# Optimization experiments

Hardware: AMD Instinct MI355X
Metric: run time of the kernel (lower is better)

The kernel has to match this reference:

```python
import jax, jax.numpy as jnp
import numpy as np

D_MODEL = 1024
NUM_HEADS = 16
D_K = D_MODEL // NUM_HEADS


def setup_inputs() -> dict:
    key = jax.random.key(0)
    ks = jax.random.split(key, 9)
    s = 1.0 / np.sqrt(D_MODEL)
    x = jax.random.normal(ks[0], (4, 2048, D_MODEL), dtype=jnp.float32)
    Wq = jax.random.uniform(ks[1], (D_MODEL, D_MODEL), jnp.float32, -s, s)
    bq = jax.random.uniform(ks[2], (D_MODEL,), jnp.float32, -s, s)
    Wk = jax.random.uniform(ks[3], (D_MODEL, D_MODEL), jnp.float32, -s, s)
    bk = jax.random.uniform(ks[4], (D_MODEL,), jnp.float32, -s, s)
    Wv = jax.random.uniform(ks[5], (D_MODEL, D_MODEL), jnp.float32, -s, s)
    bv = jax.random.uniform(ks[6], (D_MODEL,), jnp.float32, -s, s)
    Wo = jax.random.uniform(ks[7], (D_MODEL, D_MODEL), jnp.float32, -s, s)
    bo = jax.random.uniform(ks[8], (D_MODEL,), jnp.float32, -s, s)
    return {"x": x, "Wq": Wq, "bq": bq, "Wk": Wk, "bk": bk,
            "Wv": Wv, "bv": bv, "Wo": Wo, "bo": bo}


def reference(x, Wq, bq, Wk, bk, Wv, bv, Wo, bo):
    B, S, _ = x.shape
    # Linear projections (torch Linear: x @ W.T + b)
    q = x @ Wq.T + bq
    k = x @ Wk.T + bk
    v = x @ Wv.T + bv
    # [B, H, S, d_k]
    q = q.reshape(B, S, NUM_HEADS, D_K).transpose(0, 2, 1, 3)
    k = k.reshape(B, S, NUM_HEADS, D_K).transpose(0, 2, 1, 3)
    v = v.reshape(B, S, NUM_HEADS, D_K).transpose(0, 2, 1, 3)
    score = jnp.einsum('bhqd,bhkd->bhqk', q, k) / jnp.sqrt(jnp.float32(D_K))
    causal = jnp.tril(jnp.ones((S, S), dtype=bool))  # True = keep
    score = jnp.where(causal[None, None], score, -jnp.inf)
    attn = jax.nn.softmax(score, axis=-1)
    out = jnp.einsum('bhqk,bhkd->bhqd', attn, v)
    out = out.transpose(0, 2, 1, 3).reshape(B, S, D_MODEL)
    return out @ Wo.T + bo
```

## Files before the change

kernel.cpp:

```cpp
#include <hip/hip_runtime.h>
#include <hip/hip_bf16.h>
#include <stdint.h>

#define D_MODEL 1024
#define SEQ     2048
#define BATCH   4
#define NHEAD   16
#define DKH     64
#define MTOT    (BATCH * SEQ)

typedef __bf16 bf16x8 __attribute__((ext_vector_type(8)));
typedef __bf16 bf16x4 __attribute__((ext_vector_type(4)));
typedef float  floatx4 __attribute__((ext_vector_type(4)));
typedef short  s16x4  __attribute__((ext_vector_type(4)));

#define GLOAD_LDS16(gp, lp)                                            \
    __builtin_amdgcn_global_load_lds(                                  \
        (const __attribute__((address_space(1))) unsigned int*)(gp),   \
        (__attribute__((address_space(3))) unsigned int*)(lp), 16, 0, 0)

#define MFMA16(a, b, c) __builtin_amdgcn_mfma_f32_16x16x32_bf16(a, b, c, 0, 0, 0)

#if __has_builtin(__builtin_amdgcn_exp2f)
#define EXP2(x) __builtin_amdgcn_exp2f(x)
#else
#define EXP2(x) exp2f(x)
#endif

static __device__ __forceinline__ floatx4 pv_mfma(s16x4 a, s16x4 b, floatx4 c)
{
#if __has_builtin(__builtin_amdgcn_mfma_f32_16x16x16bf16_1k)
    return __builtin_amdgcn_mfma_f32_16x16x16bf16_1k(a, b, c, 0, 0, 0);
#else
    asm("v_mfma_f32_16x16x16_bf16 %0, %1, %2, %0" : "+v"(c) : "v"(a), "v"(b));
    return c;
#endif
}

__global__ __launch_bounds__(256)
void cvt_x_kernel(const float* __restrict__ src, __bf16* __restrict__ dst)
{
    const int i = (blockIdx.x * 256 + threadIdx.x) * 4;
    floatx4 v = *(const floatx4*)(src + i);
    bf16x4 o;
    o[0] = (__bf16)v[0]; o[1] = (__bf16)v[1]; o[2] = (__bf16)v[2]; o[3] = (__bf16)v[3];
    *(bf16x4*)(dst + i) = o;
}

__global__ __launch_bounds__(256)
void cvt_w3_kernel(const float* __restrict__ Wq, const float* __restrict__ Wk,
                   const float* __restrict__ Wv, __bf16* __restrict__ Wcat)
{
    const int z = blockIdx.y;
    const float* src = (z == 0) ? Wq : ((z == 1) ? Wk : Wv);
    const int i = (blockIdx.x * 256 + threadIdx.x) * 4;
    floatx4 v = *(const floatx4*)(src + i);
    bf16x4 o;
    o[0] = (__bf16)v[0]; o[1] = (__bf16)v[1]; o[2] = (__bf16)v[2]; o[3] = (__bf16)v[3];
    *(bf16x4*)(Wcat + (size_t)z * (D_MODEL * D_MODEL) + i) = o;
}

__global__ __launch_bounds__(256)
void qkv_gemm_kernel(const __bf16* __restrict__ xb, const __bf16* __restrict__ Wcat,
                     const float* __restrict__ bq, const float* __restrict__ bk,
                     const float* __restrict__ bv,
                     __bf16* __restrict__ Q, __bf16* __restrict__ K,
                     __bf16* __restrict__ Vt)
{
    __shared__ __align__(16) char smem_raw[128 * 136 * 2];
    __bf16* As = (__bf16*)smem_raw;
    __bf16* Bs = (__bf16*)(smem_raw + 8192);
    __bf16* Cs = (__bf16*)smem_raw;

    const int t    = threadIdx.x;
    const int w    = t >> 6, l = t & 63, quad = l >> 4, r16 = l & 15;
    const int wm   = w & 1, wn = w >> 1;
    const int m0   = blockIdx.y * 128;
    const int n0   = blockIdx.x * 128;
    const int z    = n0 >> 10;
    const float* bias = (z == 0) ? bq : ((z == 1) ? bk : bv);
    __bf16* outQK     = (z == 0) ? Q  : K;
    const float scale = (z == 0) ? 0.18033688011112042f : 1.0f;

    floatx4 acc[4][4];
#pragma unroll
    for (int i = 0; i < 4; ++i)
#pragma unroll
        for (int j = 0; j < 4; ++j) acc[i][j] = (floatx4){0.f, 0.f, 0.f, 0.f};

    const int c0 = t, c1 = t + 256;
    const __bf16* Ag0 = xb   + (size_t)(m0 + (c0 >> 2)) * 1024 + (c0 & 3) * 8;
    const __bf16* Ag1 = xb   + (size_t)(m0 + (c1 >> 2)) * 1024 + (c1 & 3) * 8;
    const __bf16* Bg0 = Wcat + (size_t)(n0 + (c0 >> 2)) * 1024 + (c0 & 3) * 8;
    const __bf16* Bg1 = Wcat + (size_t)(n0 + (c1 >> 2)) * 1024 + (c1 & 3) * 8;
    unsigned int* lAs = (unsigned int*)As;
    unsigned int* lBs = (unsigned int*)Bs;

    for (int k0 = 0; k0 < 1024; k0 += 32) {
        __syncthreads();
        GLOAD_LDS16(Ag0 + k0, lAs + c0 * 4);
        GLOAD_LDS16(Ag1 + k0, lAs + c1 * 4);
        GLOAD_LDS16(Bg0 + k0, lBs + c0 * 4);
        GLOAD_LDS16(Bg1 + k0, lBs + c1 * 4);
        __syncthreads();

        bf16x8 af[4], bfm[4];
#pragma unroll
        for (int i = 0; i < 4; ++i)
            af[i] = *(const bf16x8*)&As[(wm * 64 + i * 16 + r16) * 32 + quad * 8];
#pragma unroll
        for (int j = 0; j < 4; ++j)
            bfm[j] = *(const bf16x8*)&Bs[(wn * 64 + j * 16 + r16) * 32 + quad * 8];
#pragma unroll
        for (int i = 0; i < 4; ++i)
#pragma unroll
            for (int j = 0; j < 4; ++j)
                acc[i][j] = MFMA16(af[i], bfm[j], acc[i][j]);
    }

    __syncthreads();

    if (z == 2) {
#pragma unroll
        for (int i = 0; i < 4; ++i) {
            const int mb = wm * 64 + i * 16 + quad * 4;
#pragma unroll
            for (int j = 0; j < 4; ++j) {
                const int nl = wn * 64 + j * 16 + r16;
                const float bb = bias[(n0 + nl) & 1023];
                bf16x4 p4;
#pragma unroll
                for (int r = 0; r < 4; ++r) p4[r] = (__bf16)(acc[i][j][r] + bb);
                *(bf16x4*)&Cs[nl * 136 + mb] = p4;
            }
        }
    } else {
#pragma unroll
        for (int i = 0; i < 4; ++i) {
            const int mb = wm * 64 + i * 16 + quad * 4;
#pragma unroll
            for (int j = 0; j < 4; ++j) {
                const int nl = wn * 64 + j * 16 + r16;
                const float bb = bias[(n0 + nl) & 1023];
#pragma unroll
                for (int r = 0; r < 4; ++r)
                    Cs[(mb + r) * 136 + nl] =
                        (__bf16)((acc[i][j][r] + bb) * scale);
            }
        }
    }
    __syncthreads();

    const int b  = m0 >> 11;
    if (z == 2) {
#pragma unroll
        for (int k = 0; k < 8; ++k) {
            const int nl = (t >> 4) + k * 16;
            const int ml = (t & 15) * 8;
            bf16x8 row = *(const bf16x8*)&Cs[nl * 136 + ml];
            const int f = (n0 + nl) & 1023, h = f >> 6, d = f & 63;
            const int s = (m0 & 2047) + ml;
            *(bf16x8*)&Vt[((size_t)((b * 16 + h) * 64 + d) << 11) + s] = row;
        }
    } else {
#pragma unroll
        for (int k = 0; k < 8; ++k) {
            const int ml = (t >> 4) + k * 16;
            const int nl = (t & 15) * 8;
            bf16x8 row = *(const bf16x8*)&Cs[ml * 136 + nl];
            const int f = (n0 + nl) & 1023, h = f >> 6, d = f & 63;
            const int s = (m0 & 2047) + ml;
            *(bf16x8*)&outQK[((size_t)(b * 16 + h) << 17) + ((size_t)s << 6) + d]
                = row;
        }
    }
}

__global__ __launch_bounds__(256)
void out_gemm_kernel(const __bf16* __restrict__ A, const __bf16* __restrict__ Wob,
                     const float* __restrict__ bo, float* __restrict__ out)
{
    __shared__ __align__(16) __bf16 As[128 * 32];
    __shared__ __align__(16) __bf16 Bs[128 * 32];

    const int t    = threadIdx.x;
    const int w    = t >> 6, l = t & 63, quad = l >> 4, r16 = l & 15;
    const int wm   = w & 1, wn = w >> 1;
    const int m0   = blockIdx.y * 128;
    const int n0   = blockIdx.x * 128;

    floatx4 acc[4][4];
#pragma unroll
    for (int i = 0; i < 4; ++i)
#pragma unroll
        for (int j = 0; j < 4; ++j) acc[i][j] = (floatx4){0.f, 0.f, 0.f, 0.f};

    const int c0 = t, c1 = t + 256;
    const __bf16* Ag0 = A   + (size_t)(m0 + (c0 >> 2)) * 1024 + (c0 & 3) * 8;
    const __bf16* Ag1 = A   + (size_t)(m0 + (c1 >> 2)) * 1024 + (c1 & 3) * 8;
    const __bf16* Bg0 = Wob + (size_t)(n0 + (c0 >> 2)) * 1024 + (c0 & 3) * 8;
    const __bf16* Bg1 = Wob + (size_t)(n0 + (c1 >> 2)) * 1024 + (c1 & 3) * 8;
    unsigned int* lAs = (unsigned int*)As;
    unsigned int* lBs = (unsigned int*)Bs;

    for (int k0 = 0; k0 < 1024; k0 += 32) {
        __syncthreads();
        GLOAD_LDS16(Ag0 + k0, lAs + c0 * 4);
        GLOAD_LDS16(Ag1 + k0, lAs + c1 * 4);
        GLOAD_LDS16(Bg0 + k0, lBs + c0 * 4);
        GLOAD_LDS16(Bg1 + k0, lBs + c1 * 4);
        __syncthreads();

        bf16x8 af[4], bfm[4];
#pragma unroll
        for (int i = 0; i < 4; ++i)
            af[i] = *(const bf16x8*)&As[(wm * 64 + i * 16 + r16) * 32 + quad * 8];
#pragma unroll
        for (int j = 0; j < 4; ++j)
            bfm[j] = *(const bf16x8*)&Bs[(wn * 64 + j * 16 + r16) * 32 + quad * 8];
#pragma unroll
        for (int i = 0; i < 4; ++i)
#pragma unroll
            for (int j = 0; j < 4; ++j)
                acc[i][j] = MFMA16(af[i], bfm[j], acc[i][j]);
    }

#pragma unroll
    for (int i = 0; i < 4; ++i) {
        const int mg = m0 + wm * 64 + i * 16 + quad * 4;
#pragma unroll
        for (int j = 0; j < 4; ++j) {
            const int ng = n0 + wn * 64 + j * 16 + r16;
            const float bb = bo[ng];
#pragma unroll
            for (int r = 0; r < 4; ++r)
                out[(size_t)(mg + r) * 1024 + ng] = acc[i][j][r] + bb;
        }
    }
}

__global__ __launch_bounds__(512, 4)
void attn_kernel(const __bf16* __restrict__ Qg, const __bf16* __restrict__ Kg,
                 const __bf16* __restrict__ Vtg, __bf16* __restrict__ O)
{
    __shared__ __align__(16) __bf16 Ks[2][64 * 72];
    __shared__ __align__(16) __bf16 Vs[2][64 * 72];

    const int t    = threadIdx.x;
    const int w    = t >> 6, l = t & 63, quad = l >> 4, r16 = l & 15;
    const int bh   = blockIdx.x;
    const int qb   = blockIdx.y;
    const int qa   = 15 - qb;
    const size_t base = (size_t)bh * SEQ * DKH;
    const int g    = w >> 2;
    const int d0   = 2 * qa + g;
    const int d1   = 2 * qb + g;
    const int nkt  = 2 * qa + 2;
    const int row0 = qa * 128 + w * 16;
    const int row1 = qb * 128 + w * 16;

    const s16x4 ones16 = {(short)0x3F80, (short)0x3F80,
                          (short)0x3F80, (short)0x3F80};

    bf16x8 qf[2][2];
    qf[0][0] = *(const bf16x8*)&Qg[base + (size_t)(row0 + r16) * 64 + quad * 8];
    qf[0][1] = *(const bf16x8*)&Qg[base + (size_t)(row0 + r16) * 64 + 32 + quad * 8];
    qf[1][0] = *(const bf16x8*)&Qg[base + (size_t)(row1 + r16) * 64 + quad * 8];
    qf[1][1] = *(const bf16x8*)&Qg[base + (size_t)(row1 + r16) * 64 + 32 + quad * 8];

    floatx4 o[2][4];
#pragma unroll
    for (int mi = 0; mi < 2; ++mi)
#pragma unroll
        for (int j = 0; j < 4; ++j) o[mi][j] = (floatx4){0.f, 0.f, 0.f, 0.f};
    floatx4 osum[2];
    osum[0] = (floatx4){0.f, 0.f, 0.f, 0.f};
    osum[1] = (floatx4){0.f, 0.f, 0.f, 0.f};

    const int srow = t >> 3;
    const int sg   = (t & 7) * 8;

    bf16x8 pk = *(const bf16x8*)&Kg[base + (size_t)srow * 64 + sg];
    bf16x8 pv = *(const bf16x8*)&Vtg[base + (size_t)srow * 2048 + sg];

    for (int kt = 0; kt < nkt; ++kt) {
        __bf16* ks = Ks[kt & 1];
        __bf16* vs = Vs[kt & 1];
        *(bf16x8*)&ks[srow * 72 + sg] = pk;
        *(bf16x8*)&vs[srow * 72 + sg] = pv;
        if (kt + 1 < nkt) {
            pk = *(const bf16x8*)&Kg[base + (size_t)((kt + 1) * 64 + srow) * 64 + sg];
            pv = *(const bf16x8*)&Vtg[base + (size_t)srow * 2048 + (kt + 1) * 64 + sg];
        }
        __syncthreads();

        const bool a0 = (kt <= d0), a1 = (kt <= d1);
        if (a0) {
            __builtin_amdgcn_s_setprio(1);
            bf16x8 kf[4][2];
#pragma unroll
            for (int j = 0; j < 4; ++j) {
                kf[j][0] = *(const bf16x8*)&ks[(j * 16 + r16) * 72 + quad * 8];
                kf[j][1] = *(const bf16x8*)&ks[(j * 16 + r16) * 72 + 32 + quad * 8];
            }
#pragma unroll
            for (int j = 0; j < 4; ++j) {
                floatx4 z0 = (floatx4){0.f, 0.f, 0.f, 0.f};
                floatx4 z1 = (floatx4){0.f, 0.f, 0.f, 0.f};
                z0 = MFMA16(kf[j][0], qf[0][0], z0);
                z0 = MFMA16(kf[j][1], qf[0][1], z0);
                if (a1) {
                    z1 = MFMA16(kf[j][0], qf[1][0], z1);
                    z1 = MFMA16(kf[j][1], qf[1][1], z1);
                }

                const int kg = kt * 64 + j * 16 + quad * 4;
                bf16x4 pb0, pb1;
                if (kt < d0) {
#pragma unroll
                    for (int r = 0; r < 4; ++r)
                        pb0[r] = (__bf16)EXP2(z0[r]);
                } else {
                    const int qg0 = row0 + r16;
#pragma unroll
                    for (int r = 0; r < 4; ++r) {
                        float p = 0.f;
                        if (kg + r <= qg0) p = EXP2(z0[r]);
                        pb0[r] = (__bf16)p;
                    }
                }
                s16x4 pa0 = __builtin_bit_cast(s16x4, pb0);
                s16x4 pa1;
                if (a1) {
                    if (kt < d1) {
#pragma unroll
                        for (int r = 0; r < 4; ++r)
                            pb1[r] = (__bf16)EXP2(z1[r]);
                    } else {
                        const int qg1 = row1 + r16;
#pragma unroll
                        for (int r = 0; r < 4; ++r) {
                            float p = 0.f;
                            if (kg + r <= qg1) p = EXP2(z1[r]);
                            pb1[r] = (__bf16)p;
                        }
                    }
                    pa1 = __builtin_bit_cast(s16x4, pb1);
                }
                osum[0] = pv_mfma(pa0, ones16, osum[0]);
                if (a1) osum[1] = pv_mfma(pa1, ones16, osum[1]);
#pragma unroll
                for (int jd = 0; jd < 4; ++jd) {
                    const s16x4 vv =
                        *(const s16x4*)&vs[(jd * 16 + r16) * 72 + j * 16 + quad * 4];
                    o[0][jd] = pv_mfma(pa0, vv, o[0][jd]);
                    if (a1) o[1][jd] = pv_mfma(pa1, vv, o[1][jd]);
                }
            }
            __builtin_amdgcn_s_setprio(0);
        }
    }

    const int b = bh >> 4, h = bh & 15;
#pragma unroll
    for (int mi = 0; mi < 2; ++mi) {
        const int rowb = (mi == 0) ? row0 : row1;
#pragma unroll
        for (int r = 0; r < 4; ++r) {
            const int qrow = rowb + quad * 4 + r;
            const float inv = 1.f / osum[mi][r];
#pragma unroll
            for (int jd = 0; jd < 4; ++jd) {
                const int d = jd * 16 + r16;
                O[((size_t)(b * SEQ + qrow) * D_MODEL) + h * 64 + d] =
                    (__bf16)(o[mi][jd][r] * inv);
            }
        }
    }
}

extern "C" void kernel_launch(void* const* d_in, const int* in_sizes, int n_in,
                              void* d_out, int out_size, void* d_ws, size_t ws_size,
                              hipStream_t stream)
{
    (void)in_sizes; (void)n_in; (void)out_size; (void)ws_size;
    const float* x  = (const float*)d_in[0];
    const float* Wq = (const float*)d_in[1];
    const float* bq = (const float*)d_in[2];
    const float* Wk = (const float*)d_in[3];
    const float* bk = (const float*)d_in[4];
    const float* Wv = (const float*)d_in[5];
    const float* bv = (const float*)d_in[6];
    const float* Wo = (const float*)d_in[7];
    const float* bo = (const float*)d_in[8];
    float* out = (float*)d_out;

    const size_t n_elem = (size_t)MTOT * D_MODEL;
    const int    w_n    = D_MODEL * D_MODEL;
    __bf16* Qb  = (__bf16*)d_out;
    __bf16* xb  = Qb + n_elem;
    __bf16* Kb   = (__bf16*)d_ws;
    __bf16* Vtb  = Kb + n_elem;
    __bf16* Ab   = Vtb + n_elem;
    __bf16* Wcat = Ab;
    __bf16* Wob  = Kb;

    cvt_x_kernel<<<MTOT * D_MODEL / 1024, 256, 0, stream>>>(x, xb);
    cvt_w3_kernel<<<dim3(w_n / 1024, 3), 256, 0, stream>>>(Wq, Wk, Wv, Wcat);
    qkv_gemm_kernel<<<dim3(24, 64), 256, 0, stream>>>(xb, Wcat, bq, bk, bv,
                                                      Qb, Kb, Vtb);
    attn_kernel<<<dim3(64, 8), 512, 0, stream>>>(Qb, Kb, Vtb, Ab);
    cvt_x_kernel<<<w_n / 1024, 256, 0, stream>>>(Wo, Wob);
    out_gemm_kernel<<<dim3(8, 64), 256, 0, stream>>>(Ab, Wob, bo, out);
}
```

Measured before the change: 267.7 us.

## Split attention blocks into 256-thread halves with two-tile-ahead K/V prefetch

The attention kernel now launches twice as many 256-thread blocks, each covering one 64-row half of a paired causal query tile (qa, qb), instead of 512-thread blocks covering both halves. Each block loops only up to its own diagonal, which removes the idle iterations the second half-group of waves spent waiting in the old design. K/V staging now has each thread load two rows and prefetch two tiles ahead in registers, to hide global latency with fewer threads. The trade-off is more register pressure and less K/V reuse across waves, since each tile is loaded by twice as many blocks.

```diff
diff --git a/kernel.cpp b/kernel.cpp
--- a/kernel.cpp
+++ b/kernel.cpp
@@ -239,7 +239,7 @@
     }
 }
 
-__global__ __launch_bounds__(512, 4)
+__global__ __launch_bounds__(256, 4)
 void attn_kernel(const __bf16* __restrict__ Qg, const __bf16* __restrict__ Kg,
                  const __bf16* __restrict__ Vtg, __bf16* __restrict__ O)
 {
@@ -249,15 +249,15 @@
     const int t    = threadIdx.x;
     const int w    = t >> 6, l = t & 63, quad = l >> 4, r16 = l & 15;
     const int bh   = blockIdx.x;
-    const int qb   = blockIdx.y;
-    const int qa   = 15 - qb;
+    const int y    = blockIdx.y;
+    const int p    = y >> 1, half = y & 1;
+    const int qa   = 15 - p, qb = p;
     const size_t base = (size_t)bh * SEQ * DKH;
-    const int g    = w >> 2;
-    const int d0   = 2 * qa + g;
-    const int d1   = 2 * qb + g;
-    const int nkt  = 2 * qa + 2;
-    const int row0 = qa * 128 + w * 16;
-    const int row1 = qb * 128 + w * 16;
+    const int d0   = 2 * qa + half;
+    const int d1   = 2 * qb + half;
+    const int nkt  = d0 + 1;
+    const int row0 = qa * 128 + half * 64 + w * 16;
+    const int row1 = qb * 128 + half * 64 + w * 16;
 
     const s16x4 ones16 = {(short)0x3F80, (short)0x3F80,
                           (short)0x3F80, (short)0x3F80};
@@ -280,85 +280,100 @@
     const int srow = t >> 3;
     const int sg   = (t & 7) * 8;
 
-    bf16x8 pk = *(const bf16x8*)&Kg[base + (size_t)srow * 64 + sg];
-    bf16x8 pv = *(const bf16x8*)&Vtg[base + (size_t)srow * 2048 + sg];
-
-    for (int kt = 0; kt < nkt; ++kt) {
+    bf16x8 ka[2], va[2], kb[2], vb[2];
+    ka[0] = *(const bf16x8*)&Kg[base + (size_t)srow * 64 + sg];
+    ka[1] = *(const bf16x8*)&Kg[base + (size_t)(32 + srow) * 64 + sg];
+    va[0] = *(const bf16x8*)&Vtg[base + (size_t)srow * 2048 + sg];
+    va[1] = *(const bf16x8*)&Vtg[base + (size_t)(32 + srow) * 2048 + sg];
+    kb[0] = *(const bf16x8*)&Kg[base + (size_t)(64 + srow) * 64 + sg];
+    kb[1] = *(const bf16x8*)&Kg[base + (size_t)(96 + srow) * 64 + sg];
+    vb[0] = *(const bf16x8*)&Vtg[base + (size_t)srow * 2048 + 64 + sg];
+    vb[1] = *(const bf16x8*)&Vtg[base + (size_t)(32 + srow) * 2048 + 64 + sg];
+
+    auto do_tile = [&](const int kt, bf16x8* pk, bf16x8* pv) {
         __bf16* ks = Ks[kt & 1];
         __bf16* vs = Vs[kt & 1];
-        *(bf16x8*)&ks[srow * 72 + sg] = pk;
-        *(bf16x8*)&vs[srow * 72 + sg] = pv;
-        if (kt + 1 < nkt) {
-            pk = *(const bf16x8*)&Kg[base + (size_t)((kt + 1) * 64 + srow) * 64 + sg];
-            pv = *(const bf16x8*)&Vtg[base + (size_t)srow * 2048 + (kt + 1) * 64 + sg];
+        *(bf16x8*)&ks[srow * 72 + sg] = pk[0];
+        *(bf16x8*)&ks[(32 + srow) * 72 + sg] = pk[1];
+        *(bf16x8*)&vs[srow * 72 + sg] = pv[0];
+        *(bf16x8*)&vs[(32 + srow) * 72 + sg] = pv[1];
+        if (kt + 2 < nkt) {
+            const int kr = (kt + 2) * 64;
+            pk[0] = *(const bf16x8*)&Kg[base + (size_t)(kr + srow) * 64 + sg];
+            pk[1] = *(const bf16x8*)&Kg[base + (size_t)(kr + 32 + srow) * 64 + sg];
+            pv[0] = *(const bf16x8*)&Vtg[base + (size_t)srow * 2048 + kr + sg];
+            pv[1] = *(const bf16x8*)&Vtg[base + (size_t)(32 + srow) * 2048 + kr + sg];
         }
         __syncthreads();
 
-        const bool a0 = (kt <= d0), a1 = (kt <= d1);
-        if (a0) {
-            __builtin_amdgcn_s_setprio(1);
-            bf16x8 kf[4][2];
-#pragma unroll
-            for (int j = 0; j < 4; ++j) {
-                kf[j][0] = *(const bf16x8*)&ks[(j * 16 + r16) * 72 + quad * 8];
-                kf[j][1] = *(const bf16x8*)&ks[(j * 16 + r16) * 72 + 32 + quad * 8];
-            }
-#pragma unroll
-            for (int j = 0; j < 4; ++j) {
-                floatx4 z0 = (floatx4){0.f, 0.f, 0.f, 0.f};
-                floatx4 z1 = (floatx4){0.f, 0.f, 0.f, 0.f};
-                z0 = MFMA16(kf[j][0], qf[0][0], z0);
-                z0 = MFMA16(kf[j][1], qf[0][1], z0);
-                if (a1) {
-                    z1 = MFMA16(kf[j][0], qf[1][0], z1);
-                    z1 = MFMA16(kf[j][1], qf[1][1], z1);
+        const bool a1 = (kt <= d1);
+        __builtin_amdgcn_s_setprio(1);
+        bf16x8 kf[4][2];
+#pragma unroll
+        for (int j = 0; j < 4; ++j) {
+            kf[j][0] = *(const bf16x8*)&ks[(j * 16 + r16) * 72 + quad * 8];
+            kf[j][1] = *(const bf16x8*)&ks[(j * 16 + r16) * 72 + 32 + quad * 8];
+        }
+#pragma unroll
+        for (int j = 0; j < 4; ++j) {
+            floatx4 z0 = (floatx4){0.f, 0.f, 0.f, 0.f};
+            floatx4 z1 = (floatx4){0.f, 0.f, 0.f, 0.f};
+            z0 = MFMA16(kf[j][0], qf[0][0], z0);
+            z0 = MFMA16(kf[j][1], qf[0][1], z0);
+            if (a1) {
+                z1 = MFMA16(kf[j][0], qf[1][0], z1);
+                z1 = MFMA16(kf[j][1], qf[1][1], z1);
+            }
+
+            const int kg = kt * 64 + j * 16 + quad * 4;
+            bf16x4 pb0, pb1;
+            if (kt < d0) {
+#pragma unroll
+                for (int r = 0; r < 4; ++r)
+                    pb0[r] = (__bf16)EXP2(z0[r]);
+            } else {
+                const int qg0 = row0 + r16;
+#pragma unroll
+                for (int r = 0; r < 4; ++r) {
+                    float pp = 0.f;
+                    if (kg + r <= qg0) pp = EXP2(z0[r]);
+                    pb0[r] = (__bf16)pp;
                 }
-
-                const int kg = kt * 64 + j * 16 + quad * 4;
-                bf16x4 pb0, pb1;
-                if (kt < d0) {
+            }
+            s16x4 pa0 = __builtin_bit_cast(s16x4, pb0);
+            s16x4 pa1;
+            if (a1) {
+                if (kt < d1) {
 #pragma unroll
                     for (int r = 0; r < 4; ++r)
-                        pb0[r] = (__bf16)EXP2(z0[r]);
+                        pb1[r] = (__bf16)EXP2(z1[r]);
                 } else {
-                    const int qg0 = row0 + r16;
+                    const int qg1 = row1 + r16;
 #pragma unroll
                     for (int r = 0; r < 4; ++r) {
-                        float p = 0.f;
-                        if (kg + r <= qg0) p = EXP2(z0[r]);
-                        pb0[r] = (__bf16)p;
+                        float pp = 0.f;
+                        if (kg + r <= qg1) pp = EXP2(z1[r]);
+                        pb1[r] = (__bf16)pp;
                     }
                 }
-                s16x4 pa0 = __builtin_bit_cast(s16x4, pb0);
-                s16x4 pa1;
-                if (a1) {
-                    if (kt < d1) {
-#pragma unroll
-                        for (int r = 0; r < 4; ++r)
-                            pb1[r] = (__bf16)EXP2(z1[r]);
-                    } else {
-                        const int qg1 = row1 + r16;
-#pragma unroll
-                        for (int r = 0; r < 4; ++r) {
-                            float p = 0.f;
-                            if (kg + r <= qg1) p = EXP2(z1[r]);
-                            pb1[r] = (__bf16)p;
-                        }
-                    }
-                    pa1 = __builtin_bit_cast(s16x4, pb1);
-                }
-                osum[0] = pv_mfma(pa0, ones16, osum[0]);
-                if (a1) osum[1] = pv_mfma(pa1, ones16, osum[1]);
-#pragma unroll
-                for (int jd = 0; jd < 4; ++jd) {
-                    const s16x4 vv =
-                        *(const s16x4*)&vs[(jd * 16 + r16) * 72 + j * 16 + quad * 4];
-                    o[0][jd] = pv_mfma(pa0, vv, o[0][jd]);
-                    if (a1) o[1][jd] = pv_mfma(pa1, vv, o[1][jd]);
-                }
-            }
-            __builtin_amdgcn_s_setprio(0);
-        }
+                pa1 = __builtin_bit_cast(s16x4, pb1);
+            }
+            osum[0] = pv_mfma(pa0, ones16, osum[0]);
+            if (a1) osum[1] = pv_mfma(pa1, ones16, osum[1]);
+#pragma unroll
+            for (int jd = 0; jd < 4; ++jd) {
+                const s16x4 vv =
+                    *(const s16x4*)&vs[(jd * 16 + r16) * 72 + j * 16 + quad * 4];
+                o[0][jd] = pv_mfma(pa0, vv, o[0][jd]);
+                if (a1) o[1][jd] = pv_mfma(pa1, vv, o[1][jd]);
+            }
+        }
+        __builtin_amdgcn_s_setprio(0);
+    };
+
+    for (int kt = 0; kt < nkt; kt += 2) {
+        do_tile(kt, ka, va);
+        if (kt + 1 < nkt) do_tile(kt + 1, kb, vb);
     }
 
     const int b = bh >> 4, h = bh & 15;
@@ -409,7 +424,7 @@
     cvt_w3_kernel<<<dim3(w_n / 1024, 3), 256, 0, stream>>>(Wq, Wk, Wv, Wcat);
     qkv_gemm_kernel<<<dim3(24, 64), 256, 0, stream>>>(xb, Wcat, bq, bk, bv,
                                                       Qb, Kb, Vtb);
-    attn_kernel<<<dim3(64, 8), 512, 0, stream>>>(Qb, Kb, Vtb, Ab);
+    attn_kernel<<<dim3(64, 16), 256, 0, stream>>>(Qb, Kb, Vtb, Ab);
     cvt_x_kernel<<<w_n / 1024, 256, 0, stream>>>(Wo, Wob);
     out_gemm_kernel<<<dim3(8, 64), 256, 0, stream>>>(Ab, Wob, bo, out);
 }
```

Result: slower. 303.9 us (+13.5%).
